# Performance work log

Hardware: AMD Instinct MI355X
Metric: run time of the kernel (lower is better)

Reference implementation:

```python
import jax, jax.numpy as jnp
import numpy as np

B, T, D, H = 8, 1024, 1024, 16
DH = D // H
EPS = 1e-5


def setup_inputs() -> dict:
    key = jax.random.key(0)
    ks = jax.random.split(key, 8)
    s = 0.02
    return {
        "x": jax.random.normal(ks[0], (B, T, D), dtype=jnp.float32),
        # per-head Q/K/V weights stacked: (H, in_c, d_head), applied as x @ W
        "Wq": jax.random.normal(ks[1], (H, D, DH), dtype=jnp.float32) * s,
        "Wk": jax.random.normal(ks[2], (H, D, DH), dtype=jnp.float32) * s,
        "Wv": jax.random.normal(ks[3], (H, D, DH), dtype=jnp.float32) * s,
        # FFN weights stored (in, out): y = x @ W
        "W1": jax.random.normal(ks[4], (D, D), dtype=jnp.float32) * s,
        "W2": jax.random.normal(ks[5], (D, D), dtype=jnp.float32) * s,
        "g1": jnp.ones((D,), jnp.float32),
        "b1": jnp.zeros((D,), jnp.float32),
        "g2": jnp.ones((D,), jnp.float32),
        "b2": jnp.zeros((D,), jnp.float32),
    }


def _layer_norm(x, g, b):
    m = jnp.mean(x, axis=-1, keepdims=True)
    v = jnp.mean((x - m) ** 2, axis=-1, keepdims=True)  # biased, as torch LN
    return (x - m) * jax.lax.rsqrt(v + EPS) * g + b


def reference(x, Wq, Wk, Wv, W1, W2, g1, b1, g2, b2):
    b, t, d = x.shape
    dh = Wq.shape[-1]
    q = jnp.einsum("btc,hcd->bhtd", x, Wq)
    k = jnp.einsum("btc,hcd->bhtd", x, Wk)
    v = jnp.einsum("btc,hcd->bhtd", x, Wv)
    attn = jnp.einsum("bhtd,bhsd->bhts", q, k) / (dh ** 0.5)
    # Original: attn @ ones(T,T) -> every column equals rowsum(attn);
    # softmax(dim=1) over the query axis is then constant across columns,
    # so out[t] = softmax_t(rowsum)[t] * sum_s v[s]. Same math, reduced.
    rowsum = attn.sum(axis=-1)               # (B,H,T)
    p = jax.nn.softmax(rowsum, axis=-1)      # softmax over query index t
    vsum = v.sum(axis=2)                     # (B,H,DH)
    head_out = p[..., None] * vsum[:, :, None, :]        # (B,H,T,DH)
    out = head_out.transpose(0, 2, 1, 3).reshape(b, t, d)  # concat heads
    x1 = _layer_norm(x + out, g1, b1)
    ff = jax.nn.relu(x1 @ W1) @ W2           # dropout = identity (eval)
    return _layer_norm(x1 + ff, g2, b2)
```

## Files before the change

### kernel.cpp

```cpp
#include <hip/hip_runtime.h>

#define NB 8
#define NT 1024
#define ND 1024
#define NH 16
#define NDH 64
#define NM (NB*NT)
#define LNEPS 1e-5f

typedef __attribute__((ext_vector_type(8))) __bf16 bf16x8;
typedef __attribute__((ext_vector_type(4))) float f32x4;

__global__ void transpose_to_bf16(const float* __restrict__ W, __bf16* __restrict__ WT) {
    __shared__ float tile[32][33];
    int bx = blockIdx.x * 32;
    int by = blockIdx.y * 32;
    int tx = threadIdx.x;
    int ty = threadIdx.y;
    for (int i = ty; i < 32; i += 8)
        tile[i][tx] = W[(size_t)(by + i) * ND + bx + tx];
    __syncthreads();
    for (int i = ty; i < 32; i += 8)
        WT[(size_t)(bx + i) * ND + by + tx] = (__bf16)tile[tx][i];
}

__global__ void xsum_kernel(const float* __restrict__ x, float* __restrict__ xsum) {
    int b = blockIdx.x;
    int chunk = blockIdx.y;
    int tid = threadIdx.x;
    const float4* xp = (const float4*)(x + ((size_t)b * NT + chunk * 16) * ND) + tid;
    float4 s = {0.f, 0.f, 0.f, 0.f};
    #pragma unroll
    for (int t = 0; t < 16; ++t) {
        float4 v = xp[(size_t)t * (ND / 4)];
        s.x += v.x; s.y += v.y; s.z += v.z; s.w += v.w;
    }
    float* dst = xsum + b * ND + tid * 4;
    atomicAdd(dst + 0, s.x);
    atomicAdd(dst + 1, s.y);
    atomicAdd(dst + 2, s.z);
    atomicAdd(dst + 3, s.w);
}

__global__ void head_prep(const float* __restrict__ xsum,
                          const float* __restrict__ Wq, const float* __restrict__ Wk,
                          const float* __restrict__ Wv,
                          float* __restrict__ vsum, float* __restrict__ wqk) {
    int h = blockIdx.x, b = blockIdx.y;
    int t = threadIdx.x;
    int d = t & 63, q = t >> 6;
    __shared__ float part[2][4][NDH];
    __shared__ float ks[NDH];
    const float* xs = xsum + b * ND;
    float sk = 0.f, sv = 0.f;
    for (int c = q * 256; c < q * 256 + 256; ++c) {
        float xv = xs[c];
        sk += xv * Wk[((size_t)h * ND + c) * NDH + d];
        sv += xv * Wv[((size_t)h * ND + c) * NDH + d];
    }
    part[0][q][d] = sk;
    part[1][q][d] = sv;
    __syncthreads();
    if (t < 64) {
        ks[t] = part[0][0][t] + part[0][1][t] + part[0][2][t] + part[0][3][t];
    } else if (t < 128) {
        int dd = t - 64;
        vsum[((size_t)b * NH + h) * NDH + dd] =
            part[1][0][dd] + part[1][1][dd] + part[1][2][dd] + part[1][3][dd];
    }
    __syncthreads();
    for (int c = t; c < ND; c += 256) {
        const float* wq = Wq + ((size_t)h * ND + c) * NDH;
        float s = 0.f;
        #pragma unroll 16
        for (int dd = 0; dd < NDH; ++dd) s += wq[dd] * ks[dd];
        wqk[((size_t)b * NH + h) * ND + c] = s * 0.125f;
    }
}

__global__ void rowsum_kernel(const float* __restrict__ x, const float* __restrict__ wqk,
                              float* __restrict__ rowsum) {
    int t = blockIdx.x, b = blockIdx.y;
    int tid = threadIdx.x, wid = tid >> 6, lane = tid & 63;
    const float4* xrow = (const float4*)(x + ((size_t)b * NT + t) * ND);
    float4 xv[4];
    #pragma unroll
    for (int c = 0; c < 4; ++c) xv[c] = xrow[c * 64 + lane];
    float acc[4];
    #pragma unroll
    for (int hh = 0; hh < 4; ++hh) {
        int h = wid * 4 + hh;
        const float4* wrow = (const float4*)(wqk + ((size_t)b * NH + h) * ND);
        float p = 0.f;
        #pragma unroll
        for (int c = 0; c < 4; ++c) {
            float4 wv = wrow[c * 64 + lane];
            p += xv[c].x * wv.x + xv[c].y * wv.y + xv[c].z * wv.z + xv[c].w * wv.w;
        }
        acc[hh] = p;
    }
    #pragma unroll
    for (int hh = 0; hh < 4; ++hh) {
        float p = acc[hh];
        for (int off = 32; off; off >>= 1) p += __shfl_down(p, off, 64);
        if (lane == 0) rowsum[((size_t)b * NH + wid * 4 + hh) * NT + t] = p;
    }
}

__global__ void softmax_kernel(float* __restrict__ rs) {
    int bh = blockIdx.x, tid = threadIdx.x;
    int wave = tid >> 6, lane = tid & 63;
    float* row = rs + (size_t)bh * NT;
    float4 v = ((float4*)row)[tid];
    float m = fmaxf(fmaxf(v.x, v.y), fmaxf(v.z, v.w));
    __shared__ float red[4];
    for (int off = 32; off; off >>= 1) m = fmaxf(m, __shfl_down(m, off, 64));
    if (lane == 0) red[wave] = m;
    __syncthreads();
    m = fmaxf(fmaxf(red[0], red[1]), fmaxf(red[2], red[3]));
    __syncthreads();
    float4 e;
    e.x = __expf(v.x - m); e.y = __expf(v.y - m);
    e.z = __expf(v.z - m); e.w = __expf(v.w - m);
    float s = e.x + e.y + e.z + e.w;
    for (int off = 32; off; off >>= 1) s += __shfl_down(s, off, 64);
    if (lane == 0) red[wave] = s;
    __syncthreads();
    s = red[0] + red[1] + red[2] + red[3];
    float inv = 1.f / s;
    e.x *= inv; e.y *= inv; e.z *= inv; e.w *= inv;
    ((float4*)row)[tid] = e;
}

__global__ void ln1_kernel(const float* __restrict__ x, const float* __restrict__ p,
                           const float* __restrict__ vsum,
                           const float* __restrict__ g1, const float* __restrict__ b1,
                           __bf16* __restrict__ x1b) {
    int t = blockIdx.x, b = blockIdx.y, tid = threadIdx.x;
    int wave = tid >> 6, lane = tid & 63;
    size_t rowoff = ((size_t)b * NT + t) * ND;
    float4 xv = ((const float4*)(x + rowoff))[tid];
    int h = tid >> 4;
    float pv = p[((size_t)b * NH + h) * NT + t];
    float4 vs = ((const float4*)(vsum + ((size_t)b * NH + h) * NDH))[tid & 15];
    float4 s;
    s.x = xv.x + pv * vs.x; s.y = xv.y + pv * vs.y;
    s.z = xv.z + pv * vs.z; s.w = xv.w + pv * vs.w;
    float sum = s.x + s.y + s.z + s.w;
    float sq = s.x * s.x + s.y * s.y + s.z * s.z + s.w * s.w;
    __shared__ float rs_[4], rq_[4];
    for (int off = 32; off; off >>= 1) {
        sum += __shfl_down(sum, off, 64);
        sq += __shfl_down(sq, off, 64);
    }
    if (lane == 0) { rs_[wave] = sum; rq_[wave] = sq; }
    __syncthreads();
    sum = rs_[0] + rs_[1] + rs_[2] + rs_[3];
    sq = rq_[0] + rq_[1] + rq_[2] + rq_[3];
    float mu = sum * (1.f / ND);
    float var = sq * (1.f / ND) - mu * mu;
    float rstd = rsqrtf(var + LNEPS);
    float4 g = ((const float4*)g1)[tid];
    float4 bb = ((const float4*)b1)[tid];
    union { __bf16 h4[4]; uint2 u; } pk;
    pk.h4[0] = (__bf16)((s.x - mu) * rstd * g.x + bb.x);
    pk.h4[1] = (__bf16)((s.y - mu) * rstd * g.y + bb.y);
    pk.h4[2] = (__bf16)((s.z - mu) * rstd * g.z + bb.z);
    pk.h4[3] = (__bf16)((s.w - mu) * rstd * g.w + bb.w);
    ((uint2*)(x1b + rowoff))[tid] = pk.u;
}

template <int MODE>
__global__ __launch_bounds__(256) void gemm_bf16(const __bf16* __restrict__ A,
                                                 const __bf16* __restrict__ BT,
                                                 void* __restrict__ Cout) {
    const int K = 1024, N = 1024;
    __shared__ __bf16 As[128][32];
    __shared__ __bf16 Bs[128][32];
    int m0 = blockIdx.x * 128;
    int n0 = blockIdx.y * 128;
    int tid = threadIdx.x;
    int wid = tid >> 6, lane = tid & 63;
    int wr = wid >> 1, wc = wid & 1;
    int r = lane & 15, g = lane >> 4;
    int srow = wid * 32 + (lane >> 2);
    int skoff = (lane & 3) * 8;
    const __bf16* Ag = A + (size_t)(m0 + srow) * K + skoff;
    const __bf16* Bg = BT + (size_t)(n0 + srow) * K + skoff;
    f32x4 acc[4][4] = {};
    for (int k0 = 0; k0 < K; k0 += 32) {
        __syncthreads();
        __builtin_amdgcn_global_load_lds(
            (const __attribute__((address_space(1))) unsigned int*)(Ag + k0),
            (__attribute__((address_space(3))) unsigned int*)&As[wid * 32][0], 16, 0, 0);
        __builtin_amdgcn_global_load_lds(
            (const __attribute__((address_space(1))) unsigned int*)(Ag + (size_t)16 * K + k0),
            (__attribute__((address_space(3))) unsigned int*)&As[wid * 32 + 16][0], 16, 0, 0);
        __builtin_amdgcn_global_load_lds(
            (const __attribute__((address_space(1))) unsigned int*)(Bg + k0),
            (__attribute__((address_space(3))) unsigned int*)&Bs[wid * 32][0], 16, 0, 0);
        __builtin_amdgcn_global_load_lds(
            (const __attribute__((address_space(1))) unsigned int*)(Bg + (size_t)16 * K + k0),
            (__attribute__((address_space(3))) unsigned int*)&Bs[wid * 32 + 16][0], 16, 0, 0);
        __syncthreads();
        bf16x8 af[4], bf[4];
        #pragma unroll
        for (int mf = 0; mf < 4; ++mf)
            af[mf] = *(const bf16x8*)&As[wr * 64 + mf * 16 + r][g * 8];
        #pragma unroll
        for (int nf = 0; nf < 4; ++nf)
            bf[nf] = *(const bf16x8*)&Bs[wc * 64 + nf * 16 + r][g * 8];
        #pragma unroll
        for (int mf = 0; mf < 4; ++mf)
            #pragma unroll
            for (int nf = 0; nf < 4; ++nf)
                acc[mf][nf] = __builtin_amdgcn_mfma_f32_16x16x32_bf16(af[mf], bf[nf], acc[mf][nf], 0, 0, 0);
    }
    #pragma unroll
    for (int mf = 0; mf < 4; ++mf) {
        #pragma unroll
        for (int nf = 0; nf < 4; ++nf) {
            int col = n0 + wc * 64 + nf * 16 + r;
            #pragma unroll
            for (int i = 0; i < 4; ++i) {
                int row = m0 + wr * 64 + mf * 16 + g * 4 + i;
                float v = acc[mf][nf][i];
                if (MODE == 0) {
                    v = fmaxf(v, 0.f);
                    ((__bf16*)Cout)[(size_t)row * N + col] = (__bf16)v;
                } else {
                    ((float*)Cout)[(size_t)row * N + col] = v;
                }
            }
        }
    }
}

__global__ void ln2_kernel(const __bf16* __restrict__ x1b, float* __restrict__ out,
                           const float* __restrict__ g2, const float* __restrict__ b2) {
    int t = blockIdx.x, b = blockIdx.y, tid = threadIdx.x;
    int wave = tid >> 6, lane = tid & 63;
    size_t rowoff = ((size_t)b * NT + t) * ND;
    union { __bf16 h4[4]; uint2 u; } pk;
    pk.u = ((const uint2*)(x1b + rowoff))[tid];
    float4 f = ((const float4*)(out + rowoff))[tid];
    float4 s;
    s.x = (float)pk.h4[0] + f.x; s.y = (float)pk.h4[1] + f.y;
    s.z = (float)pk.h4[2] + f.z; s.w = (float)pk.h4[3] + f.w;
    float sum = s.x + s.y + s.z + s.w;
    float sq = s.x * s.x + s.y * s.y + s.z * s.z + s.w * s.w;
    __shared__ float rs_[4], rq_[4];
    for (int off = 32; off; off >>= 1) {
        sum += __shfl_down(sum, off, 64);
        sq += __shfl_down(sq, off, 64);
    }
    if (lane == 0) { rs_[wave] = sum; rq_[wave] = sq; }
    __syncthreads();
    sum = rs_[0] + rs_[1] + rs_[2] + rs_[3];
    sq = rq_[0] + rq_[1] + rq_[2] + rq_[3];
    float mu = sum * (1.f / ND);
    float var = sq * (1.f / ND) - mu * mu;
    float rstd = rsqrtf(var + LNEPS);
    float4 g = ((const float4*)g2)[tid];
    float4 bb = ((const float4*)b2)[tid];
    float4 o;
    o.x = (s.x - mu) * rstd * g.x + bb.x;
    o.y = (s.y - mu) * rstd * g.y + bb.y;
    o.z = (s.z - mu) * rstd * g.z + bb.z;
    o.w = (s.w - mu) * rstd * g.w + bb.w;
    ((float4*)(out + rowoff))[tid] = o;
}

extern "C" void kernel_launch(void* const* d_in, const int* in_sizes, int n_in,
                              void* d_out, int out_size, void* d_ws, size_t ws_size,
                              hipStream_t stream) {
    const float* x  = (const float*)d_in[0];
    const float* Wq = (const float*)d_in[1];
    const float* Wk = (const float*)d_in[2];
    const float* Wv = (const float*)d_in[3];
    const float* W1 = (const float*)d_in[4];
    const float* W2 = (const float*)d_in[5];
    const float* g1 = (const float*)d_in[6];
    const float* b1 = (const float*)d_in[7];
    const float* g2 = (const float*)d_in[8];
    const float* b2 = (const float*)d_in[9];
    float* out = (float*)d_out;

    char* w = (char*)d_ws;
    float* xsum = (float*)w;   w += (size_t)NB * ND * 4;
    float* vsum = (float*)w;   w += (size_t)NB * NH * NDH * 4;
    float* wqk  = (float*)w;   w += (size_t)NB * NH * ND * 4;
    float* rsum = (float*)w;   w += (size_t)NB * NH * NT * 4;
    __bf16* x1b = (__bf16*)w;  w += (size_t)NM * ND * 2;
    __bf16* h1b = (__bf16*)w;  w += (size_t)NM * ND * 2;
    __bf16* w1t = (__bf16*)w;  w += (size_t)ND * ND * 2;
    __bf16* w2t = (__bf16*)w;  w += (size_t)ND * ND * 2;

    hipMemsetAsync(xsum, 0, (size_t)NB * ND * 4, stream);

    transpose_to_bf16<<<dim3(32, 32), dim3(32, 8), 0, stream>>>(W1, w1t);
    transpose_to_bf16<<<dim3(32, 32), dim3(32, 8), 0, stream>>>(W2, w2t);

    xsum_kernel<<<dim3(NB, 64), 256, 0, stream>>>(x, xsum);
    head_prep<<<dim3(NH, NB), 256, 0, stream>>>(xsum, Wq, Wk, Wv, vsum, wqk);
    rowsum_kernel<<<dim3(NT, NB), 256, 0, stream>>>(x, wqk, rsum);
    softmax_kernel<<<NB * NH, 256, 0, stream>>>(rsum);
    ln1_kernel<<<dim3(NT, NB), 256, 0, stream>>>(x, rsum, vsum, g1, b1, x1b);

    gemm_bf16<0><<<dim3(64, 8), 256, 0, stream>>>(x1b, w1t, (void*)h1b);
    gemm_bf16<1><<<dim3(64, 8), 256, 0, stream>>>(h1b, w2t, (void*)out);
    ln2_kernel<<<dim3(NT, NB), 256, 0, stream>>>(x1b, out, g2, b2);
}
```

Measured before the change: 248.4 us.

## Stage wqk in LDS for rowsum, swizzle GEMM blocks, bf16 FFN output, merge transposes

The rowsum kernel now loads each batch's full 16x1024 wqk matrix into shared memory once per block and handles 16 rows per block instead of one. This cuts repeated global reads of the weights. The GEMM remaps block indices so consecutive blocks share B tiles for better L2 reuse. The second GEMM writes its output as bf16 instead of fp32 to halve write and read traffic, at some precision cost in the LN2 residual. The two weight transposes are merged into one launch, and 64KB of LDS per rowsum block lowers its occupancy.

```diff
diff --git a/kernel.cpp b/kernel.cpp
--- a/kernel.cpp
+++ b/kernel.cpp
@@ -11,8 +11,11 @@
 typedef __attribute__((ext_vector_type(8))) __bf16 bf16x8;
 typedef __attribute__((ext_vector_type(4))) float f32x4;
 
-__global__ void transpose_to_bf16(const float* __restrict__ W, __bf16* __restrict__ WT) {
+__global__ void transpose_to_bf16(const float* __restrict__ W1, const float* __restrict__ W2,
+                                  __bf16* __restrict__ WT1, __bf16* __restrict__ WT2) {
     __shared__ float tile[32][33];
+    const float* W = blockIdx.z ? W2 : W1;
+    __bf16* WT = blockIdx.z ? WT2 : WT1;
     int bx = blockIdx.x * 32;
     int by = blockIdx.y * 32;
     int tx = threadIdx.x;
@@ -78,32 +81,38 @@
     }
 }
 
-__global__ void rowsum_kernel(const float* __restrict__ x, const float* __restrict__ wqk,
-                              float* __restrict__ rowsum) {
-    int t = blockIdx.x, b = blockIdx.y;
+__global__ __launch_bounds__(256) void rowsum_kernel(const float* __restrict__ x,
+                                                     const float* __restrict__ wqk,
+                                                     float* __restrict__ rowsum) {
+    __shared__ float wl[NH * ND];
+    int tc = blockIdx.x, b = blockIdx.y;
     int tid = threadIdx.x, wid = tid >> 6, lane = tid & 63;
-    const float4* xrow = (const float4*)(x + ((size_t)b * NT + t) * ND);
-    float4 xv[4];
+    {
+        const float4* wsrc = (const float4*)(wqk + (size_t)b * NH * ND);
+        float4* wdst = (float4*)wl;
+        #pragma unroll
+        for (int i = 0; i < 16; ++i) wdst[tid + i * 256] = wsrc[tid + i * 256];
+    }
+    __syncthreads();
+    const float4* wl4 = (const float4*)wl;
     #pragma unroll
-    for (int c = 0; c < 4; ++c) xv[c] = xrow[c * 64 + lane];
-    float acc[4];
-    #pragma unroll
-    for (int hh = 0; hh < 4; ++hh) {
-        int h = wid * 4 + hh;
-        const float4* wrow = (const float4*)(wqk + ((size_t)b * NH + h) * ND);
-        float p = 0.f;
-        #pragma unroll
-        for (int c = 0; c < 4; ++c) {
-            float4 wv = wrow[c * 64 + lane];
-            p += xv[c].x * wv.x + xv[c].y * wv.y + xv[c].z * wv.z + xv[c].w * wv.w;
+    for (int j = 0; j < 4; ++j) {
+        int t = tc * 16 + wid * 4 + j;
+        const float4* xrow = (const float4*)(x + ((size_t)b * NT + t) * ND);
+        float4 xv[4];
+        #pragma unroll
+        for (int c = 0; c < 4; ++c) xv[c] = xrow[c * 64 + lane];
+        #pragma unroll
+        for (int h = 0; h < NH; ++h) {
+            float p = 0.f;
+            #pragma unroll
+            for (int c = 0; c < 4; ++c) {
+                float4 wv = wl4[h * 256 + c * 64 + lane];
+                p += xv[c].x * wv.x + xv[c].y * wv.y + xv[c].z * wv.z + xv[c].w * wv.w;
+            }
+            for (int off = 32; off; off >>= 1) p += __shfl_down(p, off, 64);
+            if (lane == 0) rowsum[((size_t)b * NH + h) * NT + t] = p;
         }
-        acc[hh] = p;
-    }
-    #pragma unroll
-    for (int hh = 0; hh < 4; ++hh) {
-        float p = acc[hh];
-        for (int off = 32; off; off >>= 1) p += __shfl_down(p, off, 64);
-        if (lane == 0) rowsum[((size_t)b * NH + wid * 4 + hh) * NT + t] = p;
     }
 }
 
@@ -170,15 +179,17 @@
     ((uint2*)(x1b + rowoff))[tid] = pk.u;
 }
 
-template <int MODE>
+template <int RELU>
 __global__ __launch_bounds__(256) void gemm_bf16(const __bf16* __restrict__ A,
                                                  const __bf16* __restrict__ BT,
-                                                 void* __restrict__ Cout) {
+                                                 __bf16* __restrict__ Cout) {
     const int K = 1024, N = 1024;
     __shared__ __bf16 As[128][32];
     __shared__ __bf16 Bs[128][32];
-    int m0 = blockIdx.x * 128;
-    int n0 = blockIdx.y * 128;
+    int raw = blockIdx.x;
+    int swz = (raw & 7) * 64 + (raw >> 3);
+    int m0 = (swz >> 3) * 128;
+    int n0 = (swz & 7) * 128;
     int tid = threadIdx.x;
     int wid = tid >> 6, lane = tid & 63;
     int wr = wid >> 1, wc = wid & 1;
@@ -225,28 +236,27 @@
             for (int i = 0; i < 4; ++i) {
                 int row = m0 + wr * 64 + mf * 16 + g * 4 + i;
                 float v = acc[mf][nf][i];
-                if (MODE == 0) {
-                    v = fmaxf(v, 0.f);
-                    ((__bf16*)Cout)[(size_t)row * N + col] = (__bf16)v;
-                } else {
-                    ((float*)Cout)[(size_t)row * N + col] = v;
-                }
+                if (RELU) v = fmaxf(v, 0.f);
+                Cout[(size_t)row * N + col] = (__bf16)v;
             }
         }
     }
 }
 
-__global__ void ln2_kernel(const __bf16* __restrict__ x1b, float* __restrict__ out,
+__global__ void ln2_kernel(const __bf16* __restrict__ x1b, const __bf16* __restrict__ ffb,
+                           float* __restrict__ out,
                            const float* __restrict__ g2, const float* __restrict__ b2) {
     int t = blockIdx.x, b = blockIdx.y, tid = threadIdx.x;
     int wave = tid >> 6, lane = tid & 63;
     size_t rowoff = ((size_t)b * NT + t) * ND;
-    union { __bf16 h4[4]; uint2 u; } pk;
+    union { __bf16 h4[4]; uint2 u; } pk, pf;
     pk.u = ((const uint2*)(x1b + rowoff))[tid];
-    float4 f = ((const float4*)(out + rowoff))[tid];
+    pf.u = ((const uint2*)(ffb + rowoff))[tid];
     float4 s;
-    s.x = (float)pk.h4[0] + f.x; s.y = (float)pk.h4[1] + f.y;
-    s.z = (float)pk.h4[2] + f.z; s.w = (float)pk.h4[3] + f.w;
+    s.x = (float)pk.h4[0] + (float)pf.h4[0];
+    s.y = (float)pk.h4[1] + (float)pf.h4[1];
+    s.z = (float)pk.h4[2] + (float)pf.h4[2];
+    s.w = (float)pk.h4[3] + (float)pf.h4[3];
     float sum = s.x + s.y + s.z + s.w;
     float sq = s.x * s.x + s.y * s.y + s.z * s.z + s.w * s.w;
     __shared__ float rs_[4], rq_[4];
@@ -293,21 +303,21 @@
     float* rsum = (float*)w;   w += (size_t)NB * NH * NT * 4;
     __bf16* x1b = (__bf16*)w;  w += (size_t)NM * ND * 2;
     __bf16* h1b = (__bf16*)w;  w += (size_t)NM * ND * 2;
+    __bf16* ffb = (__bf16*)w;  w += (size_t)NM * ND * 2;
     __bf16* w1t = (__bf16*)w;  w += (size_t)ND * ND * 2;
     __bf16* w2t = (__bf16*)w;  w += (size_t)ND * ND * 2;
 
     hipMemsetAsync(xsum, 0, (size_t)NB * ND * 4, stream);
 
-    transpose_to_bf16<<<dim3(32, 32), dim3(32, 8), 0, stream>>>(W1, w1t);
-    transpose_to_bf16<<<dim3(32, 32), dim3(32, 8), 0, stream>>>(W2, w2t);
+    transpose_to_bf16<<<dim3(32, 32, 2), dim3(32, 8), 0, stream>>>(W1, W2, w1t, w2t);
 
     xsum_kernel<<<dim3(NB, 64), 256, 0, stream>>>(x, xsum);
     head_prep<<<dim3(NH, NB), 256, 0, stream>>>(xsum, Wq, Wk, Wv, vsum, wqk);
-    rowsum_kernel<<<dim3(NT, NB), 256, 0, stream>>>(x, wqk, rsum);
+    rowsum_kernel<<<dim3(64, NB), 256, 0, stream>>>(x, wqk, rsum);
     softmax_kernel<<<NB * NH, 256, 0, stream>>>(rsum);
     ln1_kernel<<<dim3(NT, NB), 256, 0, stream>>>(x, rsum, vsum, g1, b1, x1b);
 
-    gemm_bf16<0><<<dim3(64, 8), 256, 0, stream>>>(x1b, w1t, (void*)h1b);
-    gemm_bf16<1><<<dim3(64, 8), 256, 0, stream>>>(h1b, w2t, (void*)out);
-    ln2_kernel<<<dim3(NT, NB), 256, 0, stream>>>(x1b, out, g2, b2);
-}
+    gemm_bf16<1><<<512, 256, 0, stream>>>(x1b, w1t, h1b);
+    gemm_bf16<0><<<512, 256, 0, stream>>>(h1b, w2t, ffb);
+    ln2_kernel<<<dim3(NT, NB), 256, 0, stream>>>(x1b, ffb, out, g2, b2);
+}
```

After: 235.7 us. -5.1%, faster.
